# Performance work log

Hardware: AMD Instinct MI355X
Metric: run time of the kernel (lower is better)

## Reference

```python
import jax, jax.numpy as jnp
import numpy as np

EPS = 1e-5


def gated_graph_conv(x, edge_index, W, w_ih, w_hh, b_ih, b_hh):
    # W: [num_layers, C, C]; PyG pads input features up to out_channels C.
    N = x.shape[0]
    C = W.shape[1]
    if x.shape[1] < C:
        x = jnp.pad(x, ((0, 0), (0, C - x.shape[1])))
    src, dst = edge_index[0], edge_index[1]
    for i in range(W.shape[0]):
        m = x @ W[i]                                   # [N, C]
        agg = jax.ops.segment_sum(m[src], dst, num_segments=N)  # scatter-add aggr
        # GRUCell(agg, x)
        gi = agg @ w_ih.T + b_ih                       # [N, 3C]
        gh = x @ w_hh.T + b_hh
        ir, iz, in_ = jnp.split(gi, 3, axis=-1)
        hr, hz, hn = jnp.split(gh, 3, axis=-1)
        r = jax.nn.sigmoid(ir + hr)
        z = jax.nn.sigmoid(iz + hz)
        n = jnp.tanh(in_ + r * hn)
        x = (1.0 - z) * n + z * x
    return x


def batch_norm_eval(x, gamma, beta, mean, var):
    return (x - mean) * jax.lax.rsqrt(var + EPS) * gamma + beta


def _ggc_params(key, C):
    ks = jax.random.split(key, 5)
    s = 1.0 / np.sqrt(C)
    return (jax.random.uniform(ks[0], (4, C, C), minval=-s, maxval=s),
            jax.random.uniform(ks[1], (3 * C, C), minval=-s, maxval=s),
            jax.random.uniform(ks[2], (3 * C, C), minval=-s, maxval=s),
            jax.random.uniform(ks[3], (3 * C,), minval=-s, maxval=s),
            jax.random.uniform(ks[4], (3 * C,), minval=-s, maxval=s))


def _bn_params(key, C):
    ks = jax.random.split(key, 4)
    return (jax.random.normal(ks[0], (C,)) * 0.1 + 1.0,
            jax.random.normal(ks[1], (C,)) * 0.1,
            jax.random.normal(ks[2], (C,)) * 0.1,
            jax.random.uniform(ks[3], (C,), minval=0.5, maxval=1.5))


def setup_inputs() -> dict:
    key = jax.random.key(0)
    N, E, NF, NG, NA = 50000, 800000, 32, 256, 10
    ks = jax.random.split(key, 12)
    x = jax.random.normal(ks[0], (N, NF), dtype=jnp.float32)
    edge_index = jax.random.randint(ks[1], (2, E), 0, N, dtype=jnp.int64)
    batch = jnp.sort(jax.random.randint(ks[2], (N,), 0, NG, dtype=jnp.int64))
    c1 = _ggc_params(ks[3], NF)
    c2 = _ggc_params(ks[4], 64)
    c3 = _ggc_params(ks[5], 128)
    bn1 = _bn_params(ks[6], NF)
    bn2 = _bn_params(ks[7], 64)
    s1 = 1.0 / np.sqrt(128)
    fc1_W = jax.random.uniform(ks[8], (256, 128), minval=-s1, maxval=s1)
    fc1_b = jax.random.uniform(ks[9], (256,), minval=-s1, maxval=s1)
    s2 = 1.0 / np.sqrt(256)
    fc2_W = jax.random.uniform(ks[10], (NA, 256), minval=-s2, maxval=s2)
    fc2_b = jax.random.uniform(ks[11], (NA,), minval=-s2, maxval=s2)
    d = {"x": x, "edge_index": edge_index, "batch": batch,
         "fc1_W": fc1_W, "fc1_b": fc1_b, "fc2_W": fc2_W, "fc2_b": fc2_b}
    for name, p in (("conv1", c1), ("conv2", c2), ("conv3", c3)):
        d[name + "_W"], d[name + "_wih"], d[name + "_whh"], d[name + "_bih"], d[name + "_bhh"] = p
    for name, p in (("bn1", bn1), ("bn2", bn2)):
        d[name + "_gamma"], d[name + "_beta"], d[name + "_mean"], d[name + "_var"] = p
    return d


def reference(x, edge_index, batch,
              conv1_W, conv1_wih, conv1_whh, conv1_bih, conv1_bhh,
              conv2_W, conv2_wih, conv2_whh, conv2_bih, conv2_bhh,
              conv3_W, conv3_wih, conv3_whh, conv3_bih, conv3_bhh,
              bn1_gamma, bn1_beta, bn1_mean, bn1_var,
              bn2_gamma, bn2_beta, bn2_mean, bn2_var,
              fc1_W, fc1_b, fc2_W, fc2_b):
    NUM_GRAPHS = 256
    h = jax.nn.elu(gated_graph_conv(x, edge_index, conv1_W, conv1_wih, conv1_whh, conv1_bih, conv1_bhh))
    h = batch_norm_eval(h, bn1_gamma, bn1_beta, bn1_mean, bn1_var)
    h = jax.nn.elu(gated_graph_conv(h, edge_index, conv2_W, conv2_wih, conv2_whh, conv2_bih, conv2_bhh))
    h = batch_norm_eval(h, bn2_gamma, bn2_beta, bn2_mean, bn2_var)
    h = jax.nn.elu(gated_graph_conv(h, edge_index, conv3_W, conv3_wih, conv3_whh, conv3_bih, conv3_bhh))
    g = jax.ops.segment_sum(h, batch, num_segments=NUM_GRAPHS)  # global_add_pool
    g = jax.nn.elu(g @ fc1_W.T + fc1_b)
    # dropout is identity in eval mode
    return jax.nn.log_softmax(g @ fc2_W.T + fc2_b, axis=-1)
```

## Files before the change

### kernel.cpp

```cpp
#include <hip/hip_runtime.h>
#include <math.h>


#define EPS_BN 1e-5f

typedef short short8 __attribute__((ext_vector_type(8)));
typedef unsigned short u16x8 __attribute__((ext_vector_type(8)));
typedef float f32x4 __attribute__((ext_vector_type(4)));

__device__ __forceinline__ float elu_f(float v) {
    return v > 0.f ? v : expm1f(v);
}
__device__ __forceinline__ float sigmoid_f(float v) {
    return 1.f / (1.f + __expf(-v));
}
__device__ __forceinline__ float tanh_f(float v) {
    float e = __expf(2.f * v);
    return 1.f - 2.f / (e + 1.f);
}
__device__ __forceinline__ unsigned short f2bf(float f) {
    unsigned u = __float_as_uint(f);
    unsigned r = (u + 0x7FFF + ((u >> 16) & 1)) >> 16;
    return (unsigned short)r;
}
__device__ __forceinline__ float bf2f(unsigned short b) {
    return __uint_as_float(((unsigned)b) << 16);
}
__device__ __forceinline__ void put_hl(unsigned short* __restrict__ hi,
                                       unsigned short* __restrict__ lo,
                                       size_t idx, float v) {
    unsigned short h = f2bf(v);
    hi[idx] = h;
    lo[idx] = f2bf(v - bf2f(h));
}


__global__ __launch_bounds__(256) void hist_kernel(
    const int* __restrict__ ei, int* __restrict__ deg, int E) {
    int e = blockIdx.x * 256 + threadIdx.x;
    if (e < E) atomicAdd(&deg[ei[E + e]], 1);
}

__global__ __launch_bounds__(256) void scan1_kernel(
    const int* __restrict__ deg, int* __restrict__ out,
    int* __restrict__ blockSums, int N) {
    __shared__ int sdata[256];
    int b = blockIdx.x, t = threadIdx.x;
    int base = b * 1024 + t * 4;
    int v[4], s = 0;
#pragma unroll
    for (int i = 0; i < 4; ++i) {
        v[i] = (base + i < N) ? deg[base + i] : 0;
        s += v[i];
    }
    sdata[t] = s;
    __syncthreads();
    for (int off = 1; off < 256; off <<= 1) {
        int x = (t >= off) ? sdata[t - off] : 0;
        __syncthreads();
        sdata[t] += x;
        __syncthreads();
    }
    int run = sdata[t] - s;
#pragma unroll
    for (int i = 0; i < 4; ++i) {
        if (base + i < N) out[base + i] = run;
        run += v[i];
    }
    if (t == 255) blockSums[b] = sdata[255];
}

__global__ void scan2_kernel(int* blockSums, int nb) {
    if (threadIdx.x == 0 && blockIdx.x == 0) {
        int run = 0;
        for (int i = 0; i < nb; ++i) {
            int v = blockSums[i];
            blockSums[i] = run;
            run += v;
        }
    }
}

__global__ __launch_bounds__(256) void scan3_kernel(
    const int* __restrict__ out, const int* __restrict__ blockSums,
    int* __restrict__ rowstart, int* __restrict__ writeptr, int N, int E) {
    int i = blockIdx.x * 256 + threadIdx.x;
    if (i < N) {
        int v = out[i] + blockSums[i >> 10];
        rowstart[i] = v;
        writeptr[i] = v;
    }
    if (i == 0) rowstart[N] = E;
}

__global__ __launch_bounds__(256) void fill_kernel(
    const int* __restrict__ ei, int* __restrict__ writeptr,
    int* __restrict__ csr_src, int E) {
    int e = blockIdx.x * 256 + threadIdx.x;
    if (e < E) {
        int d = ei[E + e];
        int p = atomicAdd(&writeptr[d], 1);
        csr_src[p] = ei[e];
    }
}


template <int C>
__global__ __launch_bounds__(256) void wc_kernel(
    const float* __restrict__ W, const float* __restrict__ wih,
    float* __restrict__ Wc) {
    int idx = blockIdx.x * 256 + threadIdx.x;
    if (idx >= 4 * C * 3 * C) return;
    int l = idx / (C * 3 * C);
    int r = idx % (C * 3 * C);
    int k = r / (3 * C);
    int row = r % (3 * C);
    const float* wrow = W + ((size_t)l * C + k) * C;
    const float* irow = wih + (size_t)row * C;
    float acc = 0.f;
#pragma unroll 4
    for (int t = 0; t < C; ++t) acc += wrow[t] * irow[t];
    Wc[idx] = acc;
}


template <int C>
__global__ __launch_bounds__(256) void swizzle_b2_kernel(
    const float* __restrict__ Wc, const float* __restrict__ whh,
    unsigned short* __restrict__ BsHi, unsigned short* __restrict__ BsLo) {
    constexpr int CT = C / 16;
    int idx = blockIdx.x * 256 + threadIdx.x;
    if (idx >= 4 * 6 * C * C) return;
    int l = idx / (6 * C * C);
    int r0 = idx % (6 * C * C);
    int j = r0 & 7;
    int lane = (r0 >> 3) & 63;
    int rest = r0 >> 9;
    int tslot = rest % (3 * CT);
    int ks = rest / (3 * CT);
    int k = ks * 32 + (lane >> 4) * 8 + j;
    int g = tslot / CT;
    int lt = tslot % CT;
    int c = lt * 16 + (lane & 15);
    int row = g * C + c;
    float v = (k < C) ? Wc[((size_t)l * C + k) * 3 * C + row]
                      : whh[(size_t)row * C + (k - C)];
    unsigned short h = f2bf(v);
    BsHi[idx] = h;
    BsLo[idx] = f2bf(v - bf2f(h));
}


template <int C>
__global__ __launch_bounds__(256) void gather_kernel(
    const unsigned short* __restrict__ Xhi,
    const int* __restrict__ rowstart, const int* __restrict__ csr_src,
    unsigned short* __restrict__ Shi, int N) {
    constexpr int LPG = C / 8;
    constexpr int GPB = 256 / LPG;
    int lane = threadIdx.x % LPG;
    int grp = threadIdx.x / LPG;
    int d = blockIdx.x * GPB + grp;
    if (d >= N) return;
    int p = rowstart[d];
    int p1 = rowstart[d + 1];
    float a[8];
#pragma unroll
    for (int j = 0; j < 8; ++j) a[j] = 0.f;
    int off = lane * 8;
    for (; p + 3 < p1; p += 4) {
        int s0 = csr_src[p];
        int s1 = csr_src[p + 1];
        int s2 = csr_src[p + 2];
        int s3 = csr_src[p + 3];
        u16x8 h0 = *(const u16x8*)(Xhi + (size_t)s0 * C + off);
        u16x8 h1 = *(const u16x8*)(Xhi + (size_t)s1 * C + off);
        u16x8 h2 = *(const u16x8*)(Xhi + (size_t)s2 * C + off);
        u16x8 h3 = *(const u16x8*)(Xhi + (size_t)s3 * C + off);
#pragma unroll
        for (int j = 0; j < 8; ++j) {
            a[j] += (bf2f(h0[j]) + bf2f(h1[j])) + (bf2f(h2[j]) + bf2f(h3[j]));
        }
    }
    for (; p < p1; ++p) {
        int s0 = csr_src[p];
        u16x8 h0 = *(const u16x8*)(Xhi + (size_t)s0 * C + off);
#pragma unroll
        for (int j = 0; j < 8; ++j) a[j] += bf2f(h0[j]);
    }
    size_t base = (size_t)d * C + off;
#pragma unroll
    for (int j = 0; j < 8; ++j) Shi[base + j] = f2bf(a[j]);
}


template <int C, int NT, int MINW>
__global__ __launch_bounds__(256, MINW) void gru_mfma_kernel(
    const unsigned short* __restrict__ HinHi, const unsigned short* __restrict__ HinLo,
    unsigned short* __restrict__ HoutHi, unsigned short* __restrict__ HoutLo,
    const unsigned short* __restrict__ Shi,
    const unsigned short* __restrict__ BsHi, const unsigned short* __restrict__ BsLo,
    const float* __restrict__ biasI, const float* __restrict__ biasH, int N) {
    constexpr int CT = C / 16;
    constexpr int KS = C / 16;
    constexpr int CTW = CT / 4;
    constexpr int TPW = NT / 16;
    int wave = threadIdx.x >> 6;
    int lane = threadIdx.x & 63;
    int quad = lane >> 4;
    int l16 = lane & 15;
    int node0 = blockIdx.x * NT;
    int arow[TPW];
#pragma unroll
    for (int t = 0; t < TPW; ++t) {
        int r = node0 + t * 16 + l16;
        arow[t] = r < N ? r : N - 1;
    }
    f32x4 accR[CTW][TPW], accZ[CTW][TPW], accN[CTW][TPW], accH[CTW][TPW];
#pragma unroll
    for (int ct = 0; ct < CTW; ++ct)
#pragma unroll
        for (int t = 0; t < TPW; ++t) {
            accR[ct][t] = (f32x4){0.f, 0.f, 0.f, 0.f};
            accZ[ct][t] = (f32x4){0.f, 0.f, 0.f, 0.f};
            accN[ct][t] = (f32x4){0.f, 0.f, 0.f, 0.f};
            accH[ct][t] = (f32x4){0.f, 0.f, 0.f, 0.f};
        }
    const short8* bhi = (const short8*)BsHi;
    const short8* blo = (const short8*)BsLo;

    for (int ks = 0; ks < KS / 2; ++ks) {
        int k0 = ks * 32 + quad * 8;
        short8 ahi[TPW];
#pragma unroll
        for (int t = 0; t < TPW; ++t)
            ahi[t] = *(const short8*)(Shi + (size_t)arow[t] * C + k0);
#pragma unroll
        for (int ct = 0; ct < CTW; ++ct) {
            int ts = ks * 3 * CT + wave * CTW + ct;
            short8 bhf = bhi[(size_t)ts * 64 + lane];
            short8 blf = blo[(size_t)ts * 64 + lane];
#pragma unroll
            for (int t = 0; t < TPW; ++t) {
                accR[ct][t] = __builtin_amdgcn_mfma_f32_16x16x32_bf16(ahi[t], bhf, accR[ct][t], 0, 0, 0);
                accR[ct][t] = __builtin_amdgcn_mfma_f32_16x16x32_bf16(ahi[t], blf, accR[ct][t], 0, 0, 0);
            }
            bhf = bhi[(size_t)(ts + CT) * 64 + lane];
            blf = blo[(size_t)(ts + CT) * 64 + lane];
#pragma unroll
            for (int t = 0; t < TPW; ++t) {
                accZ[ct][t] = __builtin_amdgcn_mfma_f32_16x16x32_bf16(ahi[t], bhf, accZ[ct][t], 0, 0, 0);
                accZ[ct][t] = __builtin_amdgcn_mfma_f32_16x16x32_bf16(ahi[t], blf, accZ[ct][t], 0, 0, 0);
            }
            bhf = bhi[(size_t)(ts + 2 * CT) * 64 + lane];
            blf = blo[(size_t)(ts + 2 * CT) * 64 + lane];
#pragma unroll
            for (int t = 0; t < TPW; ++t) {
                accN[ct][t] = __builtin_amdgcn_mfma_f32_16x16x32_bf16(ahi[t], bhf, accN[ct][t], 0, 0, 0);
                accN[ct][t] = __builtin_amdgcn_mfma_f32_16x16x32_bf16(ahi[t], blf, accN[ct][t], 0, 0, 0);
            }
        }
    }
    for (int ks = KS / 2; ks < KS; ++ks) {
        int k0 = ks * 32 + quad * 8 - C;
        short8 ahi[TPW], alo[TPW];
#pragma unroll
        for (int t = 0; t < TPW; ++t) {
            ahi[t] = *(const short8*)(HinHi + (size_t)arow[t] * C + k0);
            alo[t] = *(const short8*)(HinLo + (size_t)arow[t] * C + k0);
        }
#pragma unroll
        for (int ct = 0; ct < CTW; ++ct) {
            int ts = ks * 3 * CT + wave * CTW + ct;
            short8 bhf = bhi[(size_t)ts * 64 + lane];
            short8 blf = blo[(size_t)ts * 64 + lane];
#pragma unroll
            for (int t = 0; t < TPW; ++t) {
                accR[ct][t] = __builtin_amdgcn_mfma_f32_16x16x32_bf16(ahi[t], bhf, accR[ct][t], 0, 0, 0);
                accR[ct][t] = __builtin_amdgcn_mfma_f32_16x16x32_bf16(alo[t], bhf, accR[ct][t], 0, 0, 0);
                accR[ct][t] = __builtin_amdgcn_mfma_f32_16x16x32_bf16(ahi[t], blf, accR[ct][t], 0, 0, 0);
            }
            bhf = bhi[(size_t)(ts + CT) * 64 + lane];
            blf = blo[(size_t)(ts + CT) * 64 + lane];
#pragma unroll
            for (int t = 0; t < TPW; ++t) {
                accZ[ct][t] = __builtin_amdgcn_mfma_f32_16x16x32_bf16(ahi[t], bhf, accZ[ct][t], 0, 0, 0);
                accZ[ct][t] = __builtin_amdgcn_mfma_f32_16x16x32_bf16(alo[t], bhf, accZ[ct][t], 0, 0, 0);
                accZ[ct][t] = __builtin_amdgcn_mfma_f32_16x16x32_bf16(ahi[t], blf, accZ[ct][t], 0, 0, 0);
            }
            bhf = bhi[(size_t)(ts + 2 * CT) * 64 + lane];
            blf = blo[(size_t)(ts + 2 * CT) * 64 + lane];
#pragma unroll
            for (int t = 0; t < TPW; ++t) {
                accH[ct][t] = __builtin_amdgcn_mfma_f32_16x16x32_bf16(ahi[t], bhf, accH[ct][t], 0, 0, 0);
                accH[ct][t] = __builtin_amdgcn_mfma_f32_16x16x32_bf16(alo[t], bhf, accH[ct][t], 0, 0, 0);
                accH[ct][t] = __builtin_amdgcn_mfma_f32_16x16x32_bf16(ahi[t], blf, accH[ct][t], 0, 0, 0);
            }
        }
    }

#pragma unroll
    for (int ct = 0; ct < CTW; ++ct) {
        int c = (wave * CTW + ct) * 16 + l16;
        float bir = biasI[c], biz = biasI[C + c], bin = biasI[2 * C + c];
        float bhr = biasH[c], bhz = biasH[C + c], bhn = biasH[2 * C + c];
#pragma unroll
        for (int t = 0; t < TPW; ++t) {
#pragma unroll
            for (int r = 0; r < 4; ++r) {
                int node = node0 + t * 16 + quad * 4 + r;
                if (node < N) {
                    size_t gi = (size_t)node * C + c;
                    float xo = bf2f(HinHi[gi]) + bf2f(HinLo[gi]);
                    float rv = sigmoid_f(accR[ct][t][r] + bir + bhr);
                    float zv = sigmoid_f(accZ[ct][t][r] + biz + bhz);
                    float nv = tanh_f(accN[ct][t][r] + bin + rv * (accH[ct][t][r] + bhn));
                    put_hl(HoutHi, HoutLo, gi, (1.f - zv) * nv + zv * xo);
                }
            }
        }
    }
}

__global__ __launch_bounds__(256, 4) void gru32_kernel(
    const unsigned short* __restrict__ HinHi, const unsigned short* __restrict__ HinLo,
    unsigned short* __restrict__ HoutHi, unsigned short* __restrict__ HoutLo,
    const unsigned short* __restrict__ Shi,
    const unsigned short* __restrict__ BsHi, const unsigned short* __restrict__ BsLo,
    const float* __restrict__ biasI, const float* __restrict__ biasH, int N) {
    constexpr int C = 32;
    constexpr int CT = 2;
    int wave = threadIdx.x >> 6;
    int lane = threadIdx.x & 63;
    int quad = lane >> 4;
    int l16 = lane & 15;
    int node0 = blockIdx.x * 64 + wave * 16;
    int ar = node0 + l16;
    if (ar >= N) ar = N - 1;
    f32x4 accR[CT], accZ[CT], accN[CT], accH[CT];
#pragma unroll
    for (int t = 0; t < CT; ++t) {
        accR[t] = (f32x4){0.f, 0.f, 0.f, 0.f};
        accZ[t] = (f32x4){0.f, 0.f, 0.f, 0.f};
        accN[t] = (f32x4){0.f, 0.f, 0.f, 0.f};
        accH[t] = (f32x4){0.f, 0.f, 0.f, 0.f};
    }
    const short8* bhi = (const short8*)BsHi;
    const short8* blo = (const short8*)BsLo;
    int k0 = quad * 8;
    {
        short8 ahi = *(const short8*)(Shi + (size_t)ar * C + k0);
#pragma unroll
        for (int g = 0; g < 3; ++g) {
            f32x4* acc = g == 0 ? accR : (g == 1 ? accZ : accN);
#pragma unroll
            for (int t = 0; t < CT; ++t) {
                int ts = g * CT + t;
                short8 bhf = bhi[(size_t)ts * 64 + lane];
                short8 blf = blo[(size_t)ts * 64 + lane];
                acc[t] = __builtin_amdgcn_mfma_f32_16x16x32_bf16(ahi, bhf, acc[t], 0, 0, 0);
                acc[t] = __builtin_amdgcn_mfma_f32_16x16x32_bf16(ahi, blf, acc[t], 0, 0, 0);
            }
        }
    }
    {
        short8 ahi = *(const short8*)(HinHi + (size_t)ar * C + k0);
        short8 alo = *(const short8*)(HinLo + (size_t)ar * C + k0);
#pragma unroll
        for (int g = 0; g < 3; ++g) {
            f32x4* acc = g == 0 ? accR : (g == 1 ? accZ : accH);
#pragma unroll
            for (int t = 0; t < CT; ++t) {
                int ts = 3 * CT + g * CT + t;
                short8 bhf = bhi[(size_t)ts * 64 + lane];
                short8 blf = blo[(size_t)ts * 64 + lane];
                acc[t] = __builtin_amdgcn_mfma_f32_16x16x32_bf16(ahi, bhf, acc[t], 0, 0, 0);
                acc[t] = __builtin_amdgcn_mfma_f32_16x16x32_bf16(alo, bhf, acc[t], 0, 0, 0);
                acc[t] = __builtin_amdgcn_mfma_f32_16x16x32_bf16(ahi, blf, acc[t], 0, 0, 0);
            }
        }
    }
#pragma unroll
    for (int t = 0; t < CT; ++t) {
        int c = t * 16 + l16;
        float bir = biasI[c], biz = biasI[C + c], bin = biasI[2 * C + c];
        float bhr = biasH[c], bhz = biasH[C + c], bhn = biasH[2 * C + c];
#pragma unroll
        for (int r = 0; r < 4; ++r) {
            int node = node0 + quad * 4 + r;
            if (node < N) {
                size_t gi = (size_t)node * C + c;
                float xo = bf2f(HinHi[gi]) + bf2f(HinLo[gi]);
                float rv = sigmoid_f(accR[t][r] + bir + bhr);
                float zv = sigmoid_f(accZ[t][r] + biz + bhz);
                float nv = tanh_f(accN[t][r] + bin + rv * (accH[t][r] + bhn));
                put_hl(HoutHi, HoutLo, gi, (1.f - zv) * nv + zv * xo);
            }
        }
    }
}


__global__ __launch_bounds__(256) void init_x_kernel(
    const float* __restrict__ x, unsigned short* __restrict__ Hhi,
    unsigned short* __restrict__ Hlo, int total) {
    int t = blockIdx.x * 256 + threadIdx.x;
    if (t < total) put_hl(Hhi, Hlo, t, x[t]);
}

template <int Cin, int Cout>
__global__ __launch_bounds__(256) void elu_bn_pad_kernel(
    const unsigned short* __restrict__ Shi, const unsigned short* __restrict__ Slo,
    unsigned short* __restrict__ Dhi, unsigned short* __restrict__ Dlo,
    const float* __restrict__ gamma, const float* __restrict__ beta,
    const float* __restrict__ mean, const float* __restrict__ var, int N) {
    long t = (long)blockIdx.x * 256 + threadIdx.x;
    long total = (long)N * Cout;
    if (t >= total) return;
    int n = (int)(t / Cout);
    int c = (int)(t & (Cout - 1));
    float v = 0.f;
    if (c < Cin) {
        size_t si = (size_t)n * Cin + c;
        float x = bf2f(Shi[si]) + bf2f(Slo[si]);
        x = elu_f(x);
        v = (x - mean[c]) * rsqrtf(var[c] + EPS_BN) * gamma[c] + beta[c];
    }
    put_hl(Dhi, Dlo, t, v);
}

__global__ __launch_bounds__(256) void pool_elu_kernel(
    const unsigned short* __restrict__ Hhi, const unsigned short* __restrict__ Hlo,
    const int* __restrict__ batch, float* __restrict__ G, int N) {
    long t = (long)blockIdx.x * 256 + threadIdx.x;
    if (t >= (long)N * 128) return;
    int n = (int)(t >> 7);
    int c = (int)(t & 127);
    float v = elu_f(bf2f(Hhi[t]) + bf2f(Hlo[t]));
    atomicAdd(&G[batch[n] * 128 + c], v);
}

__global__ __launch_bounds__(256) void fc1_kernel(
    const float* __restrict__ G, const float* __restrict__ W,
    const float* __restrict__ b, float* __restrict__ G2) {
    __shared__ float row[128];
    int g = blockIdx.x;
    int j = threadIdx.x;
    if (j < 128) row[j] = G[g * 128 + j];
    __syncthreads();
    float acc = b[j];
    for (int k = 0; k < 128; ++k) acc += row[k] * W[j * 128 + k];
    G2[g * 256 + j] = elu_f(acc);
}

__global__ __launch_bounds__(64) void fc2_logsoftmax_kernel(
    const float* __restrict__ G2, const float* __restrict__ W,
    const float* __restrict__ b, float* __restrict__ out) {
    __shared__ float row[256];
    __shared__ float logits[10];
    __shared__ float red[2];
    int g = blockIdx.x;
    int tid = threadIdx.x;
    for (int i = tid; i < 256; i += 64) row[i] = G2[g * 256 + i];
    __syncthreads();
    if (tid < 10) {
        float acc = b[tid];
        for (int k = 0; k < 256; ++k) acc += row[k] * W[tid * 256 + k];
        logits[tid] = acc;
    }
    __syncthreads();
    if (tid == 0) {
        float m = -1e30f;
        for (int a = 0; a < 10; ++a) m = fmaxf(m, logits[a]);
        float s = 0.f;
        for (int a = 0; a < 10; ++a) s += expf(logits[a] - m);
        red[0] = m;
        red[1] = logf(s);
    }
    __syncthreads();
    if (tid < 10) out[g * 10 + tid] = logits[tid] - red[0] - red[1];
}


template <int C>
static void run_conv(unsigned short* Ahi, unsigned short* Alo,
                     unsigned short* Bhi, unsigned short* Blo,
                     unsigned short* Shi,
                     float* Wc, unsigned short* BsHi, unsigned short* BsLo,
                     const float* W, const float* wih, const float* whh,
                     const float* bih, const float* bhh,
                     const int* rowstart, const int* csr_src,
                     int N, int E, hipStream_t stream) {
    wc_kernel<C><<<(4 * C * 3 * C + 255) / 256, 256, 0, stream>>>(W, wih, Wc);
    swizzle_b2_kernel<C><<<(4 * 6 * C * C + 255) / 256, 256, 0, stream>>>(Wc, whh, BsHi, BsLo);
    constexpr int NT = (C == 128) ? 32 : 64;
    int nb = (N + NT - 1) / NT;
    constexpr int GPB = 2048 / C;
    int gblocks = (N + GPB - 1) / GPB;
    unsigned short *inHi = Ahi, *inLo = Alo, *outHi = Bhi, *outLo = Blo;
    for (int it = 0; it < 4; ++it) {
        gather_kernel<C><<<gblocks, 256, 0, stream>>>(
            inHi, rowstart, csr_src, Shi, N);
        const unsigned short* bs_h = BsHi + (size_t)it * 6 * C * C;
        const unsigned short* bs_l = BsLo + (size_t)it * 6 * C * C;
        if constexpr (C == 32)
            gru32_kernel<<<nb, 256, 0, stream>>>(
                inHi, inLo, outHi, outLo, Shi, bs_h, bs_l, bih, bhh, N);
        else
            gru_mfma_kernel<C, NT, 3><<<nb, 256, 0, stream>>>(
                inHi, inLo, outHi, outLo, Shi, bs_h, bs_l, bih, bhh, N);
        unsigned short* tp;
        tp = inHi; inHi = outHi; outHi = tp;
        tp = inLo; inLo = outLo; outLo = tp;
    }
}

extern "C" void kernel_launch(void* const* d_in, const int* in_sizes, int n_in,
                              void* d_out, int out_size, void* d_ws, size_t ws_size,
                              hipStream_t stream) {
    const float* x = (const float*)d_in[0];
    const int* ei = (const int*)d_in[1];
    const int* batch = (const int*)d_in[2];
    const float* fc1W = (const float*)d_in[3];
    const float* fc1b = (const float*)d_in[4];
    const float* fc2W = (const float*)d_in[5];
    const float* fc2b = (const float*)d_in[6];
    const float* c1W = (const float*)d_in[7];
    const float* c1wih = (const float*)d_in[8];
    const float* c1whh = (const float*)d_in[9];
    const float* c1bih = (const float*)d_in[10];
    const float* c1bhh = (const float*)d_in[11];
    const float* c2W = (const float*)d_in[12];
    const float* c2wih = (const float*)d_in[13];
    const float* c2whh = (const float*)d_in[14];
    const float* c2bih = (const float*)d_in[15];
    const float* c2bhh = (const float*)d_in[16];
    const float* c3W = (const float*)d_in[17];
    const float* c3wih = (const float*)d_in[18];
    const float* c3whh = (const float*)d_in[19];
    const float* c3bih = (const float*)d_in[20];
    const float* c3bhh = (const float*)d_in[21];
    const float* bn1g = (const float*)d_in[22];
    const float* bn1b = (const float*)d_in[23];
    const float* bn1m = (const float*)d_in[24];
    const float* bn1v = (const float*)d_in[25];
    const float* bn2g = (const float*)d_in[26];
    const float* bn2b = (const float*)d_in[27];
    const float* bn2m = (const float*)d_in[28];
    const float* bn2v = (const float*)d_in[29];

    int N = in_sizes[0] / 32;
    int E = in_sizes[1] / 2;

    const size_t NB = (size_t)N * 128;
    unsigned short* PAhi = (unsigned short*)d_ws;
    unsigned short* PAlo = PAhi + NB;
    unsigned short* PBhi = PAlo + NB;
    unsigned short* PBlo = PBhi + NB;
    unsigned short* Shi = PBlo + NB;
    unsigned short* Slo = Shi + NB;
    unsigned short* BsHi = Slo + NB;
    unsigned short* BsLo = BsHi + 393216;
    float* Wc = (float*)(BsLo + 393216);
    float* G = Wc + 196608;
    float* G2 = G + 32768;
    int* deg = (int*)(G2 + 65536);
    int* scanout = deg + N;
    int* rowstart = scanout + N;
    int* writeptr = rowstart + N + 1;
    int* blockSums = writeptr + N;
    int* csr_src = blockSums + 64;

    hipMemsetAsync(deg, 0, (size_t)N * sizeof(int), stream);
    int eblocks = (E + 255) / 256;
    hist_kernel<<<eblocks, 256, 0, stream>>>(ei, deg, E);
    int nscan = (N + 1023) / 1024;
    scan1_kernel<<<nscan, 256, 0, stream>>>(deg, scanout, blockSums, N);
    scan2_kernel<<<1, 64, 0, stream>>>(blockSums, nscan);
    scan3_kernel<<<(N + 255) / 256, 256, 0, stream>>>(scanout, blockSums, rowstart, writeptr, N, E);
    fill_kernel<<<eblocks, 256, 0, stream>>>(ei, writeptr, csr_src, E);

    init_x_kernel<<<(N * 32 + 255) / 256, 256, 0, stream>>>(x, PAhi, PAlo, N * 32);

    run_conv<32>(PAhi, PAlo, PBhi, PBlo, Shi, Wc, BsHi, BsLo,
                 c1W, c1wih, c1whh, c1bih, c1bhh, rowstart, csr_src, N, E, stream);
    elu_bn_pad_kernel<32, 64><<<(int)(((long)N * 64 + 255) / 256), 256, 0, stream>>>(
        PAhi, PAlo, PBhi, PBlo, bn1g, bn1b, bn1m, bn1v, N);

    run_conv<64>(PBhi, PBlo, PAhi, PAlo, Shi, Wc, BsHi, BsLo,
                 c2W, c2wih, c2whh, c2bih, c2bhh, rowstart, csr_src, N, E, stream);
    elu_bn_pad_kernel<64, 128><<<(int)(((long)N * 128 + 255) / 256), 256, 0, stream>>>(
        PBhi, PBlo, PAhi, PAlo, bn2g, bn2b, bn2m, bn2v, N);

    run_conv<128>(PAhi, PAlo, PBhi, PBlo, Shi, Wc, BsHi, BsLo,
                  c3W, c3wih, c3whh, c3bih, c3bhh, rowstart, csr_src, N, E, stream);

    hipMemsetAsync(G, 0, 256 * 128 * sizeof(float), stream);
    pool_elu_kernel<<<(int)(((long)N * 128 + 255) / 256), 256, 0, stream>>>(
        PAhi, PAlo, batch, G, N);

    fc1_kernel<<<256, 256, 0, stream>>>(G, fc1W, fc1b, G2);
    fc2_logsoftmax_kernel<<<256, 64, 0, stream>>>(G2, fc2W, fc2b, (float*)d_out);
}
```

Measured before the change: 931.0 us.

## Fuse per-conv gather and GRU iterations into one cooperative persistent kernel

Each graph-conv layer's four gather and GRU launches are replaced by one cooperative persistent kernel that loops over iterations and separates phases with grid-wide syncs. The grid is sized from occupancy queries and blocks stride over virtual blocks. This removes per-launch overhead and the tail gaps between the eight launches per layer, at the cost of grid.sync latency and fixed occupancy (launch bound of 3 blocks applied even to the C=32 path). The separate-launch path stays as a fallback if the cooperative launch fails.

```diff
diff --git a/kernel.cpp b/kernel.cpp
--- a/kernel.cpp
+++ b/kernel.cpp
@@ -1,5 +1,8 @@
 #include <hip/hip_runtime.h>
+#include <hip/hip_cooperative_groups.h>
 #include <math.h>
+
+namespace cg = cooperative_groups;
 
 
 #define EPS_BN 1e-5f
@@ -152,16 +155,15 @@
 
 
 template <int C>
-__global__ __launch_bounds__(256) void gather_kernel(
+__device__ __forceinline__ void gather_dev(
     const unsigned short* __restrict__ Xhi,
     const int* __restrict__ rowstart, const int* __restrict__ csr_src,
-    unsigned short* __restrict__ Shi, int N) {
+    unsigned short* __restrict__ Shi, int d0, int d1) {
     constexpr int LPG = C / 8;
-    constexpr int GPB = 256 / LPG;
     int lane = threadIdx.x % LPG;
     int grp = threadIdx.x / LPG;
-    int d = blockIdx.x * GPB + grp;
-    if (d >= N) return;
+    int d = d0 + grp;
+    if (d >= d1) return;
     int p = rowstart[d];
     int p1 = rowstart[d + 1];
     float a[8];
@@ -193,28 +195,26 @@
     for (int j = 0; j < 8; ++j) Shi[base + j] = f2bf(a[j]);
 }
 
-
-template <int C, int NT, int MINW>
-__global__ __launch_bounds__(256, MINW) void gru_mfma_kernel(
+template <int C, int TPW>
+__device__ __forceinline__ void gru_dev(
     const unsigned short* __restrict__ HinHi, const unsigned short* __restrict__ HinLo,
     unsigned short* __restrict__ HoutHi, unsigned short* __restrict__ HoutLo,
     const unsigned short* __restrict__ Shi,
     const unsigned short* __restrict__ BsHi, const unsigned short* __restrict__ BsLo,
-    const float* __restrict__ biasI, const float* __restrict__ biasH, int N) {
+    const float* __restrict__ biasI, const float* __restrict__ biasH,
+    int node0, int nlim) {
     constexpr int CT = C / 16;
     constexpr int KS = C / 16;
     constexpr int CTW = CT / 4;
-    constexpr int TPW = NT / 16;
     int wave = threadIdx.x >> 6;
     int lane = threadIdx.x & 63;
     int quad = lane >> 4;
     int l16 = lane & 15;
-    int node0 = blockIdx.x * NT;
     int arow[TPW];
 #pragma unroll
     for (int t = 0; t < TPW; ++t) {
         int r = node0 + t * 16 + l16;
-        arow[t] = r < N ? r : N - 1;
+        arow[t] = r < nlim ? r : nlim - 1;
     }
     f32x4 accR[CTW][TPW], accZ[CTW][TPW], accN[CTW][TPW], accH[CTW][TPW];
 #pragma unroll
@@ -309,7 +309,7 @@
 #pragma unroll
             for (int r = 0; r < 4; ++r) {
                 int node = node0 + t * 16 + quad * 4 + r;
-                if (node < N) {
+                if (node < nlim) {
                     size_t gi = (size_t)node * C + c;
                     float xo = bf2f(HinHi[gi]) + bf2f(HinLo[gi]);
                     float rv = sigmoid_f(accR[ct][t][r] + bir + bhr);
@@ -322,21 +322,22 @@
     }
 }
 
-__global__ __launch_bounds__(256, 4) void gru32_kernel(
+__device__ __forceinline__ void gru32_dev(
     const unsigned short* __restrict__ HinHi, const unsigned short* __restrict__ HinLo,
     unsigned short* __restrict__ HoutHi, unsigned short* __restrict__ HoutLo,
     const unsigned short* __restrict__ Shi,
     const unsigned short* __restrict__ BsHi, const unsigned short* __restrict__ BsLo,
-    const float* __restrict__ biasI, const float* __restrict__ biasH, int N) {
+    const float* __restrict__ biasI, const float* __restrict__ biasH,
+    int blk0, int nlim) {
     constexpr int C = 32;
     constexpr int CT = 2;
     int wave = threadIdx.x >> 6;
     int lane = threadIdx.x & 63;
     int quad = lane >> 4;
     int l16 = lane & 15;
-    int node0 = blockIdx.x * 64 + wave * 16;
+    int node0 = blk0 + wave * 16;
     int ar = node0 + l16;
-    if (ar >= N) ar = N - 1;
+    if (ar >= nlim) ar = nlim - 1;
     f32x4 accR[CT], accZ[CT], accN[CT], accH[CT];
 #pragma unroll
     for (int t = 0; t < CT; ++t) {
@@ -388,7 +389,7 @@
 #pragma unroll
         for (int r = 0; r < 4; ++r) {
             int node = node0 + quad * 4 + r;
-            if (node < N) {
+            if (node < nlim) {
                 size_t gi = (size_t)node * C + c;
                 float xo = bf2f(HinHi[gi]) + bf2f(HinLo[gi]);
                 float rv = sigmoid_f(accR[t][r] + bir + bhr);
@@ -398,6 +399,76 @@
             }
         }
     }
+}
+
+
+template <int C, int TPW>
+__global__ __launch_bounds__(256, 3) void conv_coop_kernel(
+    unsigned short* Ahi, unsigned short* Alo,
+    unsigned short* Bhi, unsigned short* Blo,
+    unsigned short* Shi,
+    const int* rowstart, const int* csr_src,
+    const unsigned short* BsHi, const unsigned short* BsLo,
+    const float* biasI, const float* biasH, int N) {
+    cg::grid_group grid = cg::this_grid();
+    constexpr int GPB = 2048 / C;
+    constexpr int NT = TPW * 16;
+    int gblocks = (N + GPB - 1) / GPB;
+    int rblocks = (N + NT - 1) / NT;
+    unsigned short *inHi = Ahi, *inLo = Alo, *outHi = Bhi, *outLo = Blo;
+#pragma unroll 1
+    for (int it = 0; it < 4; ++it) {
+#pragma unroll 1
+        for (int vb = blockIdx.x; vb < gblocks; vb += gridDim.x)
+            gather_dev<C>(inHi, rowstart, csr_src, Shi, vb * GPB, N);
+        grid.sync();
+        const unsigned short* bs_h = BsHi + (size_t)it * 6 * C * C;
+        const unsigned short* bs_l = BsLo + (size_t)it * 6 * C * C;
+#pragma unroll 1
+        for (int vb = blockIdx.x; vb < rblocks; vb += gridDim.x) {
+            if constexpr (C == 32)
+                gru32_dev(inHi, inLo, outHi, outLo, Shi, bs_h, bs_l,
+                          biasI, biasH, vb * NT, N);
+            else
+                gru_dev<C, TPW>(inHi, inLo, outHi, outLo, Shi, bs_h, bs_l,
+                                biasI, biasH, vb * NT, N);
+        }
+        grid.sync();
+        unsigned short* tp;
+        tp = inHi; inHi = outHi; outHi = tp;
+        tp = inLo; inLo = outLo; outLo = tp;
+    }
+}
+
+
+template <int C>
+__global__ __launch_bounds__(256) void gather_kernel(
+    const unsigned short* __restrict__ Xhi,
+    const int* __restrict__ rowstart, const int* __restrict__ csr_src,
+    unsigned short* __restrict__ Shi, int N) {
+    constexpr int GPB = 2048 / C;
+    gather_dev<C>(Xhi, rowstart, csr_src, Shi, blockIdx.x * GPB, N);
+}
+
+template <int C, int TPW>
+__global__ __launch_bounds__(256, 3) void gru_mfma_kernel(
+    const unsigned short* __restrict__ HinHi, const unsigned short* __restrict__ HinLo,
+    unsigned short* __restrict__ HoutHi, unsigned short* __restrict__ HoutLo,
+    const unsigned short* __restrict__ Shi,
+    const unsigned short* __restrict__ BsHi, const unsigned short* __restrict__ BsLo,
+    const float* __restrict__ biasI, const float* __restrict__ biasH, int N) {
+    gru_dev<C, TPW>(HinHi, HinLo, HoutHi, HoutLo, Shi, BsHi, BsLo,
+                    biasI, biasH, blockIdx.x * TPW * 16, N);
+}
+
+__global__ __launch_bounds__(256, 4) void gru32_kernel(
+    const unsigned short* __restrict__ HinHi, const unsigned short* __restrict__ HinLo,
+    unsigned short* __restrict__ HoutHi, unsigned short* __restrict__ HoutLo,
+    const unsigned short* __restrict__ Shi,
+    const unsigned short* __restrict__ BsHi, const unsigned short* __restrict__ BsLo,
+    const float* __restrict__ biasI, const float* __restrict__ biasH, int N) {
+    gru32_dev(HinHi, HinLo, HoutHi, HoutLo, Shi, BsHi, BsLo,
+              biasI, biasH, blockIdx.x * 64, N);
 }
 
 
@@ -482,7 +553,7 @@
 }
 
 
-template <int C>
+template <int C, int TPW>
 static void run_conv(unsigned short* Ahi, unsigned short* Alo,
                      unsigned short* Bhi, unsigned short* Blo,
                      unsigned short* Shi,
@@ -493,10 +564,32 @@
                      int N, int E, hipStream_t stream) {
     wc_kernel<C><<<(4 * C * 3 * C + 255) / 256, 256, 0, stream>>>(W, wih, Wc);
     swizzle_b2_kernel<C><<<(4 * 6 * C * C + 255) / 256, 256, 0, stream>>>(Wc, whh, BsHi, BsLo);
-    constexpr int NT = (C == 128) ? 32 : 64;
-    int nb = (N + NT - 1) / NT;
     constexpr int GPB = 2048 / C;
+    constexpr int NT = TPW * 16;
     int gblocks = (N + GPB - 1) / GPB;
+    int rblocks = (N + NT - 1) / NT;
+
+    static int nblk = -2;
+    if (nblk == -2) {
+        nblk = -1;
+        hipOccupancyMaxActiveBlocksPerMultiprocessor(
+            &nblk, conv_coop_kernel<C, TPW>, 256, 0);
+    }
+    if (nblk >= 1) {
+        int G = nblk * 256;
+        int maxvb = gblocks > rblocks ? gblocks : rblocks;
+        if (G > maxvb) G = maxvb;
+        unsigned short *a0 = Ahi, *a1 = Alo, *b0 = Bhi, *b1 = Blo, *s0 = Shi;
+        const int *rs = rowstart, *cs = csr_src;
+        const unsigned short *bh = BsHi, *bl = BsLo;
+        const float *bi = bih, *bhh2 = bhh;
+        int n = N;
+        void* args[] = {&a0, &a1, &b0, &b1, &s0, &rs, &cs, &bh, &bl, &bi, &bhh2, &n};
+        if (hipLaunchCooperativeKernel((const void*)conv_coop_kernel<C, TPW>,
+                                       dim3(G), dim3(256), args, 0, stream) == hipSuccess)
+            return;
+    }
+
     unsigned short *inHi = Ahi, *inLo = Alo, *outHi = Bhi, *outLo = Blo;
     for (int it = 0; it < 4; ++it) {
         gather_kernel<C><<<gblocks, 256, 0, stream>>>(
@@ -504,10 +597,10 @@
         const unsigned short* bs_h = BsHi + (size_t)it * 6 * C * C;
         const unsigned short* bs_l = BsLo + (size_t)it * 6 * C * C;
         if constexpr (C == 32)
-            gru32_kernel<<<nb, 256, 0, stream>>>(
+            gru32_kernel<<<rblocks, 256, 0, stream>>>(
                 inHi, inLo, outHi, outLo, Shi, bs_h, bs_l, bih, bhh, N);
         else
-            gru_mfma_kernel<C, NT, 3><<<nb, 256, 0, stream>>>(
+            gru_mfma_kernel<C, TPW><<<rblocks, 256, 0, stream>>>(
                 inHi, inLo, outHi, outLo, Shi, bs_h, bs_l, bih, bhh, N);
         unsigned short* tp;
         tp = inHi; inHi = outHi; outHi = tp;
@@ -582,18 +675,18 @@
 
     init_x_kernel<<<(N * 32 + 255) / 256, 256, 0, stream>>>(x, PAhi, PAlo, N * 32);
 
-    run_conv<32>(PAhi, PAlo, PBhi, PBlo, Shi, Wc, BsHi, BsLo,
-                 c1W, c1wih, c1whh, c1bih, c1bhh, rowstart, csr_src, N, E, stream);
+    run_conv<32, 4>(PAhi, PAlo, PBhi, PBlo, Shi, Wc, BsHi, BsLo,
+                    c1W, c1wih, c1whh, c1bih, c1bhh, rowstart, csr_src, N, E, stream);
     elu_bn_pad_kernel<32, 64><<<(int)(((long)N * 64 + 255) / 256), 256, 0, stream>>>(
         PAhi, PAlo, PBhi, PBlo, bn1g, bn1b, bn1m, bn1v, N);
 
-    run_conv<64>(PBhi, PBlo, PAhi, PAlo, Shi, Wc, BsHi, BsLo,
-                 c2W, c2wih, c2whh, c2bih, c2bhh, rowstart, csr_src, N, E, stream);
+    run_conv<64, 4>(PBhi, PBlo, PAhi, PAlo, Shi, Wc, BsHi, BsLo,
+                    c2W, c2wih, c2whh, c2bih, c2bhh, rowstart, csr_src, N, E, stream);
     elu_bn_pad_kernel<64, 128><<<(int)(((long)N * 128 + 255) / 256), 256, 0, stream>>>(
         PBhi, PBlo, PAhi, PAlo, bn2g, bn2b, bn2m, bn2v, N);
 
-    run_conv<128>(PAhi, PAlo, PBhi, PBlo, Shi, Wc, BsHi, BsLo,
-                  c3W, c3wih, c3whh, c3bih, c3bhh, rowstart, csr_src, N, E, stream);
+    run_conv<128, 2>(PAhi, PAlo, PBhi, PBlo, Shi, Wc, BsHi, BsLo,
+                     c3W, c3wih, c3whh, c3bih, c3bhh, rowstart, csr_src, N, E, stream);
 
     hipMemsetAsync(G, 0, 256 * 128 * sizeof(float), stream);
     pool_elu_kernel<<<(int)(((long)N * 128 + 255) / 256), 256, 0, stream>>>(
```

After: 2.700 ms. 190% more time.
